# Kernel tuning notes

Measured on AMD Instinct MI355X. Metric: run time of the kernel, lower is better.

The kernel has to match this reference:

```python
import jax, jax.numpy as jnp
import numpy as np


def _mlp(x, w1, b1, w2, b2):
    # Linear->ReLU->Linear->ReLU (torch Linear: y = x @ W.T + b)
    return jax.nn.relu(jax.nn.relu(x @ w1.T + b1) @ w2.T + b2)


def _lstm_cell(x, h, c, wih, whh, bih, bhh):
    g = x @ wih.T + bih + h @ whh.T + bhh
    i, f, gg, o = jnp.split(g, 4, axis=-1)  # torch gate order i,f,g,o
    c = jax.nn.sigmoid(f) * c + jax.nn.sigmoid(i) * jnp.tanh(gg)
    h = jax.nn.sigmoid(o) * jnp.tanh(c)
    return h, c


def _decode(iml, img_features, mlp1_w1, mlp1_b1, mlp1_w2, mlp1_b2,
            mlp2_w1, mlp2_b1, mlp2_w2, mlp2_b2,
            lstm_wih, lstm_whh, lstm_bih, lstm_bhh,
            attn_w, attn_b, fc_w, fc_b, emb, max_seq_len):
    # iml: [B, H, K] flattened conv map; annotations are channel vectors per position
    ann = jnp.transpose(iml, (0, 2, 1))          # [B, K, H]
    mean_ann = jnp.mean(iml, axis=-1)            # [B, H]
    h0 = _mlp(mean_ann, mlp1_w1, mlp1_b1, mlp1_w2, mlp1_b2)
    c0 = _mlp(mean_ann, mlp2_w1, mlp2_b1, mlp2_w2, mlp2_b2)
    H = h0.shape[-1]
    # attn = Linear(2H, 1) on cat(ann, h): decompose into two dot products.
    w_a, w_h = attn_w[:H], attn_w[H:]
    e_ann = ann @ w_a + attn_b[0]                # [B, K], annotation part precomputed

    def step(carry, _):
        x, h, c = carry
        h, c = _lstm_cell(x, h, c, lstm_wih, lstm_whh, lstm_bih, lstm_bhh)
        e = e_ann + (h @ w_h)[:, None]           # [B, K] fused concat+linear scores
        alpha = jax.nn.softmax(e, axis=-1)       # [B, K]
        cs = jnp.einsum('bk,bkh->bh', alpha, ann)  # weighted context [B, H]
        logits = jnp.concatenate([h, cs], axis=-1) @ fc_w.T + fc_b  # [B, V]
        sample = jnp.argmax(logits, axis=-1)     # greedy token
        return (emb[sample], h, c), (logits, sample)

    _, (logits, samples) = jax.lax.scan(step, (img_features, h0, c0), None, length=max_seq_len)
    # scan stacks on axis 0 (time); move to [B, T, ...]
    return jnp.transpose(logits, (1, 0, 2)), jnp.transpose(samples, (1, 0))


def setup_inputs() -> dict:
    B, K, H, E, V, T = 64, 196, 512, 512, 10000, 30
    key = jax.random.key(0)
    ks = jax.random.split(key, 11)
    inv = 1.0 / np.sqrt(H)
    r = lambda i, shape, scale=1.0: jax.random.normal(ks[i], shape, jnp.float32) * scale
    return {
        'iml': r(0, (B, H, K)),
        'img_features': r(1, (B, E)),
        'mlp1_w1': r(2, (H, H), inv), 'mlp1_b1': jnp.zeros(H, jnp.float32),
        'mlp1_w2': r(3, (H, H), inv), 'mlp1_b2': jnp.zeros(H, jnp.float32),
        'mlp2_w1': r(4, (H, H), inv), 'mlp2_b1': jnp.zeros(H, jnp.float32),
        'mlp2_w2': r(5, (H, H), inv), 'mlp2_b2': jnp.zeros(H, jnp.float32),
        'lstm_wih': r(6, (4 * H, E), inv), 'lstm_whh': r(7, (4 * H, H), inv),
        'lstm_bih': jnp.zeros(4 * H, jnp.float32), 'lstm_bhh': jnp.zeros(4 * H, jnp.float32),
        'attn_w': r(8, (2 * H,), inv), 'attn_b': jnp.zeros(1, jnp.float32),
        'fc_w': r(9, (V, 2 * H), inv), 'fc_b': jnp.zeros(V, jnp.float32),
        'emb': r(10, (V, E)),
        'max_seq_len': T,
    }


def reference(iml, img_features, mlp1_w1, mlp1_b1, mlp1_w2, mlp1_b2,
              mlp2_w1, mlp2_b1, mlp2_w2, mlp2_b2,
              lstm_wih, lstm_whh, lstm_bih, lstm_bhh,
              attn_w, attn_b, fc_w, fc_b, emb, max_seq_len):
    all_logits, sampled_ids = _decode(
        iml, img_features, mlp1_w1, mlp1_b1, mlp1_w2, mlp1_b2,
        mlp2_w1, mlp2_b1, mlp2_w2, mlp2_b2,
        lstm_wih, lstm_whh, lstm_bih, lstm_bhh,
        attn_w, attn_b, fc_w, fc_b, emb, max_seq_len)
    return all_logits, sampled_ids
```

## Files before the change

kernel.cpp:

```cpp
#include <hip/hip_runtime.h>
#include <hip/hip_bf16.h>

#define B 64
#define KDIM 196
#define H 512
#define E 512
#define V 10000
#define TSTEPS 30
#define VP 10240
#define NVC 40


__global__ void k_transpose_fc(const float* __restrict__ fcw, float* __restrict__ dst, int coloff) {
    __shared__ float tile[32][33];
    int v0 = blockIdx.x * 32, i0 = blockIdx.y * 32;
    int tx = threadIdx.x, ty = threadIdx.y;
#pragma unroll
    for (int r = 0; r < 32; r += 8) {
        int v = v0 + ty + r; int i = i0 + tx;
        tile[ty + r][tx] = (v < V) ? fcw[(size_t)v * 1024 + coloff + i] : 0.f;
    }
    __syncthreads();
#pragma unroll
    for (int r = 0; r < 32; r += 8) {
        int i = i0 + ty + r; int v = v0 + tx;
        dst[(size_t)i * VP + v] = tile[tx][ty + r];
    }
}

__global__ void k_build_wct(const float* __restrict__ wih, const float* __restrict__ whh,
                            float* __restrict__ dst) {
    __shared__ float tile[32][33];
    int j0 = blockIdx.x * 32, i0 = blockIdx.y * 32;
    int tx = threadIdx.x, ty = threadIdx.y;
#pragma unroll
    for (int r = 0; r < 32; r += 8) {
        int j = j0 + ty + r; int i = i0 + tx;
        tile[ty + r][tx] = (i < 512) ? wih[(size_t)j * 512 + i] : whh[(size_t)j * 512 + i - 512];
    }
    __syncthreads();
#pragma unroll
    for (int r = 0; r < 32; r += 8) {
        int i = i0 + ty + r; int j = j0 + tx;
        dst[(size_t)i * 2048 + j] = tile[tx][ty + r];
    }
}

__global__ void k_mean(const float* __restrict__ iml, float* __restrict__ mean) {
    int w = threadIdx.x >> 6, lane = threadIdx.x & 63;
    int row = blockIdx.x * 4 + w;
    const float* p = iml + (size_t)row * KDIM;
    float s = p[lane] + p[lane + 64] + p[lane + 128] + ((lane < 4) ? p[lane + 192] : 0.f);
#pragma unroll
    for (int off = 32; off; off >>= 1) s += __shfl_down(s, off);
    if (lane == 0) mean[row] = s * (1.f / 196.f);
}

__global__ void k_e_alpha(const float* __restrict__ iml, const float* __restrict__ attn_w,
                          float* __restrict__ alpha) {
    int b = blockIdx.x, t = threadIdx.x;
    __shared__ float wa[512];
    wa[t] = attn_w[t]; wa[t + 256] = attn_w[t + 256];
    __syncthreads();
    float acc = 0.f;
    if (t < KDIM) {
        const float* p = iml + (size_t)b * 512 * KDIM + t;
#pragma unroll 8
        for (int h = 0; h < 512; ++h) acc += p[(size_t)h * KDIM] * wa[h];
    }
    __shared__ float red[256];
    red[t] = (t < KDIM) ? acc : -__builtin_inff();
    __syncthreads();
    for (int s = 128; s; s >>= 1) { if (t < s) red[t] = fmaxf(red[t], red[t + s]); __syncthreads(); }
    float mx = red[0];
    __syncthreads();
    float ex = (t < KDIM) ? expf(acc - mx) : 0.f;
    red[t] = ex; __syncthreads();
    for (int s = 128; s; s >>= 1) { if (t < s) red[t] += red[t + s]; __syncthreads(); }
    if (t < KDIM) alpha[b * KDIM + t] = ex / red[0];
}

__global__ void k_cs(const float* __restrict__ iml, const float* __restrict__ alpha,
                     float* __restrict__ cs) {
    int w = threadIdx.x >> 6, lane = threadIdx.x & 63;
    int row = blockIdx.x * 4 + w;
    int b = row >> 9;
    const float* p = iml + (size_t)row * KDIM;
    const float* al = alpha + b * KDIM;
    float s = p[lane] * al[lane] + p[lane + 64] * al[lane + 64] + p[lane + 128] * al[lane + 128]
            + ((lane < 4) ? p[lane + 192] * al[lane + 192] : 0.f);
#pragma unroll
    for (int off = 32; off; off >>= 1) s += __shfl_down(s, off);
    if (lane == 0) cs[row] = s;
}

__global__ void k_dense_relu(const float* __restrict__ in, const float* __restrict__ W,
                             const float* __restrict__ bias, float* __restrict__ out, int ostride) {
    int b = blockIdx.y; int j = blockIdx.x * 256 + threadIdx.x;
    __shared__ float xs[512];
    xs[threadIdx.x] = in[b * 512 + threadIdx.x];
    xs[threadIdx.x + 256] = in[b * 512 + threadIdx.x + 256];
    __syncthreads();
    float acc = bias[j];
    const float4* w4 = (const float4*)(W + (size_t)j * 512);
#pragma unroll 4
    for (int i4 = 0; i4 < 128; ++i4) {
        float4 w = w4[i4];
        float4 x = *(const float4*)&xs[i4 * 4];
        acc += w.x * x.x + w.y * x.y + w.z * x.z + w.w * x.w;
    }
    out[(size_t)b * ostride + j] = fmaxf(acc, 0.f);
}

__global__ void k_init_xh(const float* __restrict__ img, float* __restrict__ xh) {
    int b = blockIdx.x, tid = threadIdx.x;
    ((float4*)(xh + (size_t)b * 1024))[tid] = ((const float4*)(img + (size_t)b * 512))[tid];
}

__global__ void k_gemm_big(const float* __restrict__ A, int astride,
                           const float* __restrict__ Wt, int wn,
                           float* __restrict__ part) {
    int jb = blockIdx.x, kc = blockIdx.y, bh = blockIdx.z;
    int w = threadIdx.x >> 6, lane = threadIdx.x & 63;
    int b0 = __builtin_amdgcn_readfirstlane(bh * 32 + w * 8);
    int k0 = kc * 64;
    int j0 = jb * 256 + lane * 4;
    float4 acc[8];
#pragma unroll
    for (int b = 0; b < 8; ++b) acc[b] = make_float4(0.f, 0.f, 0.f, 0.f);
    const float* wp = Wt + (size_t)k0 * wn + j0;
    const float* xp = A + (size_t)b0 * astride + k0;
#pragma unroll 8
    for (int kk = 0; kk < 64; ++kk) {
        float4 w4 = *(const float4*)(wp + (size_t)kk * wn);
#pragma unroll
        for (int b = 0; b < 8; ++b) {
            float xv = xp[(size_t)b * astride + kk];
            acc[b].x += xv * w4.x; acc[b].y += xv * w4.y;
            acc[b].z += xv * w4.z; acc[b].w += xv * w4.w;
        }
    }
#pragma unroll
    for (int b = 0; b < 8; ++b)
        *(float4*)(part + (size_t)(kc * 64 + b0 + b) * wn + j0) = acc[b];
}


__global__ void k_gates(const float* __restrict__ part, const float* __restrict__ bih,
                        const float* __restrict__ bhh, float* __restrict__ xh,
                        float* __restrict__ cbuf) {
    int e = blockIdx.x * 256 + threadIdx.x;
    int b = e >> 9, jj = e & 511;
    float g[4];
#pragma unroll
    for (int gg = 0; gg < 4; ++gg) {
        int j = jj + gg * 512;
        float s = bih[j] + bhh[j];
#pragma unroll
        for (int c = 0; c < 16; ++c) s += part[(size_t)(c * 64 + b) * 2048 + j];
        g[gg] = s;
    }
    float ig = 1.f / (1.f + expf(-g[0]));
    float fg = 1.f / (1.f + expf(-g[1]));
    float gt = tanhf(g[2]);
    float og = 1.f / (1.f + expf(-g[3]));
    float c = fg * cbuf[e] + ig * gt;
    float h = og * tanhf(c);
    cbuf[e] = c;
    xh[(size_t)b * 1024 + 512 + jj] = h;
}

__global__ void k_base_finish(const float* __restrict__ lpart, const float* __restrict__ fc_b,
                              float* __restrict__ base) {
    int b = blockIdx.y; int v = blockIdx.x * 256 + threadIdx.x;
    if (v < V) {
        float s = fc_b[v];
#pragma unroll
        for (int c = 0; c < 8; ++c) s += lpart[(size_t)(c * 64 + b) * VP + v];
        base[(size_t)b * VP + v] = s;
    }
}

__global__ void k_logits_finish(const float* __restrict__ lpart, const float* __restrict__ base,
                                float* __restrict__ out0, float* __restrict__ amaxv,
                                int* __restrict__ amaxi, int t) {
    int b = blockIdx.y, vc = blockIdx.x, tid = threadIdx.x;
    int v = vc * 256 + tid;
    float val = -__builtin_inff();
    if (v < V) {
        float s = base[(size_t)b * VP + v];
#pragma unroll
        for (int c = 0; c < 8; ++c) s += lpart[(size_t)(c * 64 + b) * VP + v];
        out0[((size_t)b * TSTEPS + t) * V + v] = s;
        val = s;
    }
    __shared__ float sv[256]; __shared__ int si[256];
    sv[tid] = val; si[tid] = (v < V) ? v : 0x7fffffff;
    __syncthreads();
    for (int s = 128; s; s >>= 1) {
        if (tid < s) {
            if (sv[tid + s] > sv[tid] || (sv[tid + s] == sv[tid] && si[tid + s] < si[tid])) {
                sv[tid] = sv[tid + s]; si[tid] = si[tid + s];
            }
        }
        __syncthreads();
    }
    if (tid == 0) { amaxv[b * NVC + vc] = sv[0]; amaxi[b * NVC + vc] = si[0]; }
}

__global__ void k_argmax_gather(const float* __restrict__ amaxv, const int* __restrict__ amaxi,
                                const float* __restrict__ emb, float* __restrict__ xh,
                                float* __restrict__ out1, int t) {
    int b = blockIdx.x, tid = threadIdx.x;
    __shared__ float sv[64]; __shared__ int si[64];
    if (tid < 64) {
        sv[tid] = (tid < NVC) ? amaxv[b * NVC + tid] : -__builtin_inff();
        si[tid] = (tid < NVC) ? amaxi[b * NVC + tid] : 0x7fffffff;
    }
    __syncthreads();
    for (int s = 32; s; s >>= 1) {
        if (tid < s) {
            if (sv[tid + s] > sv[tid] || (sv[tid + s] == sv[tid] && si[tid + s] < si[tid])) {
                sv[tid] = sv[tid + s]; si[tid] = si[tid + s];
            }
        }
        __syncthreads();
    }
    int bi = si[0];
    ((float4*)(xh + (size_t)b * 1024))[tid] = ((const float4*)(emb + (size_t)bi * 512))[tid];
    if (tid == 0) out1[b * TSTEPS + t] = (float)bi;
}


extern "C" void kernel_launch(void* const* d_in, const int* in_sizes, int n_in,
                              void* d_out, int out_size, void* d_ws, size_t ws_size,
                              hipStream_t stream) {
    const float* iml   = (const float*)d_in[0];
    const float* img   = (const float*)d_in[1];
    const float* m1w1  = (const float*)d_in[2];
    const float* m1b1  = (const float*)d_in[3];
    const float* m1w2  = (const float*)d_in[4];
    const float* m1b2  = (const float*)d_in[5];
    const float* m2w1  = (const float*)d_in[6];
    const float* m2b1  = (const float*)d_in[7];
    const float* m2w2  = (const float*)d_in[8];
    const float* m2b2  = (const float*)d_in[9];
    const float* wih   = (const float*)d_in[10];
    const float* whh   = (const float*)d_in[11];
    const float* bih   = (const float*)d_in[12];
    const float* bhh   = (const float*)d_in[13];
    const float* attnw = (const float*)d_in[14];
    const float* fcw   = (const float*)d_in[16];
    const float* fcb   = (const float*)d_in[17];
    const float* emb   = (const float*)d_in[18];

    float* out0 = (float*)d_out;
    float* out1 = out0 + (size_t)B * TSTEPS * V;

    float* ws = (float*)d_ws;
    size_t off = 0;
    float* fcT   = ws + off; off += (size_t)512 * VP;
    float* WcT   = ws + off; off += (size_t)1024 * 2048;
    float* bigp  = ws + off; off += (size_t)8 * B * VP;
    float* base  = ws + off; off += (size_t)B * VP;
    float* xh    = ws + off; off += (size_t)B * 1024;
    float* meanb = ws + off; off += B * 512;
    float* alpha = ws + off; off += B * KDIM;
    float* csb   = ws + off; off += B * 512;
    float* tmpb  = ws + off; off += B * 512;
    float* cbuf  = ws + off; off += B * 512;
    float* amaxv = ws + off; off += B * NVC;
    int*   amaxi = (int*)(ws + off); off += B * NVC;

    k_mean<<<dim3(8192), dim3(256), 0, stream>>>(iml, meanb);
    k_e_alpha<<<dim3(64), dim3(256), 0, stream>>>(iml, attnw, alpha);
    k_cs<<<dim3(8192), dim3(256), 0, stream>>>(iml, alpha, csb);
    k_dense_relu<<<dim3(2, 64), dim3(256), 0, stream>>>(meanb, m1w1, m1b1, tmpb, 512);
    k_dense_relu<<<dim3(2, 64), dim3(256), 0, stream>>>(tmpb, m1w2, m1b2, xh + 512, 1024);
    k_dense_relu<<<dim3(2, 64), dim3(256), 0, stream>>>(meanb, m2w1, m2b1, tmpb, 512);
    k_dense_relu<<<dim3(2, 64), dim3(256), 0, stream>>>(tmpb, m2w2, m2b2, cbuf, 512);
    k_init_xh<<<dim3(64), dim3(128), 0, stream>>>(img, xh);

    k_transpose_fc<<<dim3(VP / 32, 16), dim3(32, 8), 0, stream>>>(fcw, fcT, 512);
    k_gemm_big<<<dim3(40, 8, 2), dim3(256), 0, stream>>>(csb, 512, fcT, VP, bigp);
    k_base_finish<<<dim3(NVC, 64), dim3(256), 0, stream>>>(bigp, fcb, base);
    k_transpose_fc<<<dim3(VP / 32, 16), dim3(32, 8), 0, stream>>>(fcw, fcT, 0);
    k_build_wct<<<dim3(64, 32), dim3(32, 8), 0, stream>>>(wih, whh, WcT);

    for (int t = 0; t < TSTEPS; ++t) {
        k_gemm_big<<<dim3(8, 16, 2), dim3(256), 0, stream>>>(xh, 1024, WcT, 2048, bigp);
        k_gates<<<dim3(128), dim3(256), 0, stream>>>(bigp, bih, bhh, xh, cbuf);
        k_gemm_big<<<dim3(40, 8, 2), dim3(256), 0, stream>>>(xh + 512, 1024, fcT, VP, bigp);
        k_logits_finish<<<dim3(NVC, 64), dim3(256), 0, stream>>>(bigp, base, out0, amaxv, amaxi, t);
        k_argmax_gather<<<dim3(64), dim3(128), 0, stream>>>(amaxv, amaxi, emb, xh, out1, t);
    }
}
```

Before: 1.223 ms.

## Fuse per-step logits GEMM, bias add and block argmax into one kernel

```diff
diff --git a/kernel.cpp b/kernel.cpp
--- a/kernel.cpp
+++ b/kernel.cpp
@@ -181,31 +181,48 @@
     }
 }
 
-__global__ void k_logits_finish(const float* __restrict__ lpart, const float* __restrict__ base,
-                                float* __restrict__ out0, float* __restrict__ amaxv,
-                                int* __restrict__ amaxi, int t) {
-    int b = blockIdx.y, vc = blockIdx.x, tid = threadIdx.x;
-    int v = vc * 256 + tid;
-    float val = -__builtin_inff();
-    if (v < V) {
-        float s = base[(size_t)b * VP + v];
-#pragma unroll
-        for (int c = 0; c < 8; ++c) s += lpart[(size_t)(c * 64 + b) * VP + v];
-        out0[((size_t)b * TSTEPS + t) * V + v] = s;
-        val = s;
-    }
-    __shared__ float sv[256]; __shared__ int si[256];
-    sv[tid] = val; si[tid] = (v < V) ? v : 0x7fffffff;
-    __syncthreads();
-    for (int s = 128; s; s >>= 1) {
-        if (tid < s) {
-            if (sv[tid + s] > sv[tid] || (sv[tid + s] == sv[tid] && si[tid + s] < si[tid])) {
-                sv[tid] = sv[tid + s]; si[tid] = si[tid + s];
-            }
+__global__ __launch_bounds__(256) void k_logits_fused(
+        const float* __restrict__ xh, const float* __restrict__ fcT,
+        const float* __restrict__ base, float* __restrict__ out0,
+        float* __restrict__ amaxv, int* __restrict__ amaxi, int t) {
+    int jb = blockIdx.x, bh = blockIdx.y;
+    int w = threadIdx.x >> 6, lane = threadIdx.x & 63;
+    int b0 = __builtin_amdgcn_readfirstlane(bh * 8 + w * 2);
+    int j0 = jb * 256 + lane * 4;
+    const float* wp = fcT + j0;
+    const float* x0 = xh + (size_t)b0 * 1024 + 512;
+    const float* x1 = x0 + 1024;
+    float4 a0 = make_float4(0.f, 0.f, 0.f, 0.f);
+    float4 a1 = make_float4(0.f, 0.f, 0.f, 0.f);
+#pragma unroll 8
+    for (int kk = 0; kk < 512; ++kk) {
+        float4 w4 = *(const float4*)(wp + (size_t)kk * VP);
+        float v0 = x0[kk], v1 = x1[kk];
+        a0.x += v0 * w4.x; a0.y += v0 * w4.y; a0.z += v0 * w4.z; a0.w += v0 * w4.w;
+        a1.x += v1 * w4.x; a1.y += v1 * w4.y; a1.z += v1 * w4.z; a1.w += v1 * w4.w;
+    }
+#pragma unroll
+    for (int u = 0; u < 2; ++u) {
+        int b = b0 + u;
+        float4 acc = u ? a1 : a0;
+        float m; int mi;
+        if (j0 < V) {
+            float4 bs = *(const float4*)(base + (size_t)b * VP + j0);
+            float4 val = make_float4(acc.x + bs.x, acc.y + bs.y, acc.z + bs.z, acc.w + bs.w);
+            *(float4*)(out0 + ((size_t)b * TSTEPS + t) * V + j0) = val;
+            m = val.x; mi = j0;
+            if (val.y > m) { m = val.y; mi = j0 + 1; }
+            if (val.z > m) { m = val.z; mi = j0 + 2; }
+            if (val.w > m) { m = val.w; mi = j0 + 3; }
+        } else { m = -__builtin_inff(); mi = 0x7fffffff; }
+#pragma unroll
+        for (int mk = 1; mk < 64; mk <<= 1) {
+            float ov = __shfl_xor(m, mk);
+            int oi = __shfl_xor(mi, mk);
+            if (ov > m || (ov == m && oi < mi)) { m = ov; mi = oi; }
         }
-        __syncthreads();
-    }
-    if (tid == 0) { amaxv[b * NVC + vc] = sv[0]; amaxi[b * NVC + vc] = si[0]; }
+        if (lane == 0) { amaxv[b * NVC + jb] = m; amaxi[b * NVC + jb] = mi; }
+    }
 }
 
 __global__ void k_argmax_gather(const float* __restrict__ amaxv, const int* __restrict__ amaxi,
@@ -290,8 +307,7 @@
     for (int t = 0; t < TSTEPS; ++t) {
         k_gemm_big<<<dim3(8, 16, 2), dim3(256), 0, stream>>>(xh, 1024, WcT, 2048, bigp);
         k_gates<<<dim3(128), dim3(256), 0, stream>>>(bigp, bih, bhh, xh, cbuf);
-        k_gemm_big<<<dim3(40, 8, 2), dim3(256), 0, stream>>>(xh + 512, 1024, fcT, VP, bigp);
-        k_logits_finish<<<dim3(NVC, 64), dim3(256), 0, stream>>>(bigp, base, out0, amaxv, amaxi, t);
+        k_logits_fused<<<dim3(40, 8), dim3(256), 0, stream>>>(xh, fcT, base, out0, amaxv, amaxi, t);
         k_argmax_gather<<<dim3(64), dim3(128), 0, stream>>>(amaxv, amaxi, emb, xh, out1, t);
     }
 }
```

Result: slower. 1.627 ms (+33.0%).
